# Performance work log

Hardware: AMD Instinct MI355X
Metric: run time of the kernel (lower is better)

Reference implementation:

```python
import math
import jax, jax.numpy as jnp
import numpy as np

N_FEATURES = 32
DEGREE = 3
BATCH = 8192
N_POLY = math.comb(N_FEATURES + DEGREE, DEGREE)  # 6545


def _build_monomial_indices(n_features, degree):
    """Static (numpy) indices replicating the Pascal-triangle recursion in TaylorMap._poly.

    For degree level i (i = 1..degree-1), the original code appends, for each feature f,
    x[:, f] * prev_block[:, :comb(i+f, i)].  We flatten that into gather index arrays so the
    whole block is one vectorized gather+multiply instead of a Python loop of slices/concats.
    """
    levels = []
    for i in range(1, degree):
        counts = np.array([math.comb(i + f, i) for f in range(n_features)], dtype=np.int64)
        f_idx = np.repeat(np.arange(n_features, dtype=np.int64), counts)
        m_idx = np.concatenate([np.arange(c, dtype=np.int64) for c in counts])
        levels.append((f_idx, m_idx))
    return levels

_LEVELS = _build_monomial_indices(N_FEATURES, DEGREE)


def _poly(x):
    # x: [B, n].  Returns [B, n_poly] monomial features in the exact order of TaylorMap._poly.
    b = x.shape[0]
    parts = [jnp.ones((b, 1), x.dtype), x]
    prev = x
    for f_idx, m_idx in _LEVELS:  # static loop over degree levels (degree-1 iterations)
        new = x[:, f_idx] * prev[:, m_idx]  # [B, comb(n+i, i+1)-ish block]
        parts.append(new)
        prev = new
    return jnp.concatenate(parts, axis=-1)


def setup_inputs() -> dict:
    key = jax.random.key(0)
    kx, kw = jax.random.split(key)
    x = jax.random.normal(kx, (BATCH, N_FEATURES), dtype=jnp.float32)
    # learned weight W: [n_poly, n_features] (default init is zeros; use small randn for a
    # non-degenerate numerical baseline)
    W = jax.random.normal(kw, (N_POLY, N_FEATURES), dtype=jnp.float32) * 0.02
    return {"x": x, "W": W}


def reference(x, W):
    # TaylorMap(x) = x * residual + poly(x) @ W   (residual=True)
    return x + _poly(x) @ W
```

## Files before the change

### kernel.cpp

```cpp
#include <hip/hip_runtime.h>
#include <cstdint>
#include <cstddef>
#include <utility>


#define NF 32
#define NPOLY 6545
#define NSTEPS 417
#define NOCT 834
#define TSTRIDE 576
#define D2OFF 40
#define XDSTRIDE 34

typedef _Float16 f16x8 __attribute__((ext_vector_type(8)));
typedef float f32x16 __attribute__((ext_vector_type(16)));

#define D2N 528
struct D2I { uint8_t a[D2N]; uint8_t b[D2N]; };
constexpr D2I build_d2i() {
    D2I t{};
    int k = 0;
    for (int f = 0; f < NF; ++f)
        for (int m = 0; m <= f; ++m) { t.a[k] = (uint8_t)f; t.b[k] = (uint8_t)m; ++k; }
    return t;
}
constexpr D2I D2T = build_d2i();

struct Desc { uint32_t d[NOCT]; };
constexpr Desc build_desc() {
    Desc D{};
    int u = 0;
    for (int o = 0; o < 72; ++o)
        D.d[u++] = (uint32_t)(o * 8);
    for (int f = 0; f < NF; ++f) {
        int cnt = (f + 1) * (f + 2) / 2;
        for (int j8 = 0; j8 < (cnt + 7) / 8; ++j8)
            D.d[u++] = (uint32_t)(D2OFF + 8 * j8) | ((uint32_t)(1 + f) << 16);
    }
    return D;
}
__device__ const Desc DESC_G = build_desc();

struct Oldk { int16_t v[NSTEPS * 16]; };
constexpr Oldk build_oldk() {
    Oldk K{};
    int k = 0;
    for (int ti = 0; ti < 576; ++ti) {
        int old;
        if (ti == 0) old = 0;
        else if (ti <= 32) old = ti;
        else if (ti >= D2OFF && ti < D2OFF + D2N) old = 33 + (ti - D2OFF);
        else old = -1;
        K.v[k++] = (int16_t)old;
    }
    for (int f = 0; f < NF; ++f) {
        int cnt = (f + 1) * (f + 2) / 2;
        int off3 = 0;
        for (int g = 0; g < f; ++g) off3 += (g + 1) * (g + 2) / 2;
        int oc = (cnt + 7) / 8;
        for (int m = 0; m < oc * 8; ++m)
            K.v[k++] = (int16_t)(m < cnt ? 561 + off3 + m : -1);
    }
    return K;
}
__device__ const Oldk OLDK_G = build_oldk();

template<int TI>
__device__ __forceinline__ _Float16 tval(const float (&xr)[NF]) {
    if constexpr (TI == 0) return (_Float16)1.0f;
    else if constexpr (TI >= 1 && TI <= 32) return (_Float16)xr[TI - 1];
    else if constexpr (TI >= D2OFF && TI < D2OFF + D2N) {
        constexpr int m = TI - D2OFF;
        return (_Float16)(xr[D2T.a[m]] * xr[D2T.b[m]]);
    } else return (_Float16)0.0f;
}

template<int O, int... Js>
__device__ __forceinline__ void put_oct(std::integer_sequence<int, Js...>,
                                        const float (&xr)[NF], _Float16* trow, int r) {
    f16x8 v = { tval<O * 8 + Js>(xr)... };
    int slot = (O & ~7) | ((O ^ r) & 7);
    *(f16x8*)(trow + slot * 8) = v;
}

template<int V>
__device__ __forceinline__ void xdw(const float (&xr)[NF], _Float16* xdrow) {
    if constexpr (V == 0) xdrow[0] = (_Float16)1.0f;
    else xdrow[V] = (_Float16)xr[V - 1];
}

template<int G, int... Os>
__device__ __forceinline__ void p1_group(std::integer_sequence<int, Os...>,
                                         const float (&xr)[NF], _Float16* trow,
                                         _Float16* xdrow, int r) {
    (put_oct<9 * G + Os>(std::make_integer_sequence<int, 8>{}, xr, trow, r), ...);
    xdw<4 * G + 0>(xr, xdrow); xdw<4 * G + 1>(xr, xdrow);
    xdw<4 * G + 2>(xr, xdrow); xdw<4 * G + 3>(xr, xdrow);
    if constexpr (G == 7) xdw<32>(xr, xdrow);
}

__global__ void prep(const float* __restrict__ x, const float* __restrict__ W,
                     float* __restrict__ out, _Float16* __restrict__ Wh) {
    int b = blockIdx.x;
    if (b < 256) {
        int id = b * 256 + threadIdx.x;
        ((float4*)out)[id] = ((const float4*)x)[id];
    } else {
        int id = (b - 256) * 256 + threadIdx.x;
        if (id < NSTEPS * 2 * 32) {
            int step = id >> 6, rem = id & 63, hs = rem >> 5, n = rem & 31;
            int k0 = step * 16 + hs * 8;
            f16x8 v;
#pragma unroll
            for (int j = 0; j < 8; ++j) {
                int old = OLDK_G.v[k0 + j];
                v[j] = (_Float16)(old >= 0 ? W[old * 32 + n] : 0.0f);
            }
            *(f16x8*)(Wh + (size_t)id * 8) = v;
        }
    }
}

__global__ __launch_bounds__(256) void gemm(const float* __restrict__ x,
                                            const _Float16* __restrict__ Wh,
                                            float* __restrict__ out) {
    __shared__ __align__(16) unsigned char smem[39040];
    _Float16* t  = (_Float16*)smem;
    _Float16* xd = (_Float16*)(smem + 36864);
    float* red   = (float*)smem;

    const int tid = threadIdx.x;
    const int wave = tid >> 6, lane = tid & 63;
    const int hsel = lane >> 5, r = lane & 31;
    const int mtile = blockIdx.x >> 2, cg = blockIdx.x & 3;

    {
        const int pr = tid & 31, g = tid >> 5;
        float xr[NF];
        const float4* xp = (const float4*)(x + (size_t)(mtile * 32 + pr) * NF);
#pragma unroll
        for (int i = 0; i < 8; ++i) {
            float4 v = xp[i];
            xr[4 * i + 0] = v.x; xr[4 * i + 1] = v.y;
            xr[4 * i + 2] = v.z; xr[4 * i + 3] = v.w;
        }
        _Float16* trow = t + pr * TSTRIDE;
        _Float16* xdrow = xd + pr * XDSTRIDE;
        switch (g) {
            case 0: p1_group<0>(std::make_integer_sequence<int, 9>{}, xr, trow, xdrow, pr); break;
            case 1: p1_group<1>(std::make_integer_sequence<int, 9>{}, xr, trow, xdrow, pr); break;
            case 2: p1_group<2>(std::make_integer_sequence<int, 9>{}, xr, trow, xdrow, pr); break;
            case 3: p1_group<3>(std::make_integer_sequence<int, 9>{}, xr, trow, xdrow, pr); break;
            case 4: p1_group<4>(std::make_integer_sequence<int, 9>{}, xr, trow, xdrow, pr); break;
            case 5: p1_group<5>(std::make_integer_sequence<int, 9>{}, xr, trow, xdrow, pr); break;
            case 6: p1_group<6>(std::make_integer_sequence<int, 9>{}, xr, trow, xdrow, pr); break;
            default: p1_group<7>(std::make_integer_sequence<int, 9>{}, xr, trow, xdrow, pr); break;
        }
    }
    __syncthreads();

    const int c = cg * 4 + wave;
    const int s0 = __builtin_amdgcn_readfirstlane((c * NSTEPS) >> 4);
    const int s1 = __builtin_amdgcn_readfirstlane(((c + 1) * NSTEPS) >> 4);
    const _Float16* trow = t + r * TSTRIDE;
    const _Float16* xdrow = xd + r * XDSTRIDE;
    const _Float16* wp = Wh + (size_t)lane * 8;

    f32x16 acc;
#pragma unroll
    for (int i = 0; i < 16; ++i) acc[i] = 0.0f;

    uint32_t dlo = DESC_G.d[2 * s0];
    uint32_t dhi = DESC_G.d[2 * s0 + 1];
    f16x8 b0 = *(const f16x8*)(wp + (size_t)s0 * 512);
    f16x8 b1 = *(const f16x8*)(wp + (size_t)(s0 + 1) * 512);

    for (int s = s0; s < s1; ++s) {
        uint32_t d = hsel ? dhi : dlo;
        dlo = DESC_G.d[2 * (s + 1)];
        dhi = DESC_G.d[2 * (s + 1) + 1];
        int toff = (int)(d & 0xffffu);
        int xv = (int)(d >> 16);
        int o = toff >> 3;
        int slot = (o & ~7) | ((o ^ r) & 7);
        f16x8 araw = *(const f16x8*)(trow + slot * 8);
        _Float16 xs = xdrow[xv];
        f16x8 xsv = { xs, xs, xs, xs, xs, xs, xs, xs };
        f16x8 a = araw * xsv;
        f16x8 bu = b0; b0 = b1;
        b1 = *(const f16x8*)(wp + (size_t)(s + 2) * 512);
        acc = __builtin_amdgcn_mfma_f32_32x32x16_f16(a, bu, acc, 0, 0, 0);
    }

    __syncthreads();
    float* bank = red + wave * 1024;
#pragma unroll
    for (int reg = 0; reg < 16; ++reg) {
        int rr = (reg & 3) + 8 * (reg >> 2) + 4 * hsel;
        bank[rr * 32 + r] = acc[reg];
    }
    __syncthreads();
    float* op = out + (size_t)mtile * 1024;
#pragma unroll
    for (int i = 0; i < 4; ++i) {
        int e = tid + i * 256;
        float v = red[e] + red[1024 + e] + red[2048 + e] + red[3072 + e];
        atomicAdd(op + e, v);
    }
}

extern "C" void kernel_launch(void* const* d_in, const int* in_sizes, int n_in,
                              void* d_out, int out_size, void* d_ws, size_t ws_size,
                              hipStream_t stream) {
    (void)in_sizes; (void)n_in; (void)out_size; (void)ws_size;
    const float* x = (const float*)d_in[0];
    const float* W = (const float*)d_in[1];
    float* out = (float*)d_out;
    _Float16* Wh = (_Float16*)d_ws;

    prep<<<361, 256, 0, stream>>>(x, W, out, Wh);
    gemm<<<1024, 256, 0, stream>>>(x, Wh, out);
}
```

Baseline: 74.23 us.

## Use one 512-thread block per M-tile, drop atomics, stage descriptors in LDS

The K-split moves from four 256-thread blocks per 32-row tile to a single 512-thread block whose eight waves each take a K slice. Their partials are reduced in LDS and written directly as x plus the sum, which removes the global atomics and the x-to-out copy in the prep kernel. Step descriptors are staged in LDS with byte offsets precomputed. The MFMA loop now alternates two accumulators with deeper software prefetch of A, the scale factor and B. The trade-off is 256 blocks instead of 1024, which lowers grid-level parallelism, and the polynomial tile is rebuilt once per block instead of once per K-group.

```diff
diff --git a/kernel.cpp b/kernel.cpp
--- a/kernel.cpp
+++ b/kernel.cpp
@@ -8,9 +8,17 @@
 #define NPOLY 6545
 #define NSTEPS 417
 #define NOCT 834
+#define NDESC 842
 #define TSTRIDE 576
 #define D2OFF 40
 #define XDSTRIDE 34
+
+#define T_BYTES   36864
+#define XD_OFF    36864
+#define XD_BYTES  2176
+#define DESC_OFF  39040
+#define DESC_BYTES 3368
+#define SMEM_BYTES 42496
 
 typedef _Float16 f16x8 __attribute__((ext_vector_type(8)));
 typedef float f32x16 __attribute__((ext_vector_type(16)));
@@ -31,11 +39,11 @@
     Desc D{};
     int u = 0;
     for (int o = 0; o < 72; ++o)
-        D.d[u++] = (uint32_t)(o * 8);
+        D.d[u++] = (uint32_t)(o * 16);
     for (int f = 0; f < NF; ++f) {
         int cnt = (f + 1) * (f + 2) / 2;
         for (int j8 = 0; j8 < (cnt + 7) / 8; ++j8)
-            D.d[u++] = (uint32_t)(D2OFF + 8 * j8) | ((uint32_t)(1 + f) << 16);
+            D.d[u++] = (uint32_t)((D2OFF + 8 * j8) * 2) | ((uint32_t)((1 + f) * 2) << 16);
     }
     return D;
 }
@@ -83,56 +91,58 @@
     *(f16x8*)(trow + slot * 8) = v;
 }
 
+template<int BASE, int... Os>
+__device__ __forceinline__ void p1_octs(std::integer_sequence<int, Os...>,
+                                        const float (&xr)[NF], _Float16* trow, int r) {
+    (put_oct<BASE + Os>(std::make_integer_sequence<int, 8>{}, xr, trow, r), ...);
+}
+
 template<int V>
 __device__ __forceinline__ void xdw(const float (&xr)[NF], _Float16* xdrow) {
     if constexpr (V == 0) xdrow[0] = (_Float16)1.0f;
-    else xdrow[V] = (_Float16)xr[V - 1];
-}
-
-template<int G, int... Os>
-__device__ __forceinline__ void p1_group(std::integer_sequence<int, Os...>,
-                                         const float (&xr)[NF], _Float16* trow,
+    else if constexpr (V <= 32) xdrow[V] = (_Float16)xr[V - 1];
+}
+
+template<int G>
+__device__ __forceinline__ void p1_group(const float (&xr)[NF], _Float16* trow,
                                          _Float16* xdrow, int r) {
-    (put_oct<9 * G + Os>(std::make_integer_sequence<int, 8>{}, xr, trow, r), ...);
-    xdw<4 * G + 0>(xr, xdrow); xdw<4 * G + 1>(xr, xdrow);
-    xdw<4 * G + 2>(xr, xdrow); xdw<4 * G + 3>(xr, xdrow);
-    if constexpr (G == 7) xdw<32>(xr, xdrow);
-}
-
-__global__ void prep(const float* __restrict__ x, const float* __restrict__ W,
-                     float* __restrict__ out, _Float16* __restrict__ Wh) {
-    int b = blockIdx.x;
-    if (b < 256) {
-        int id = b * 256 + threadIdx.x;
-        ((float4*)out)[id] = ((const float4*)x)[id];
-    } else {
-        int id = (b - 256) * 256 + threadIdx.x;
-        if (id < NSTEPS * 2 * 32) {
-            int step = id >> 6, rem = id & 63, hs = rem >> 5, n = rem & 31;
-            int k0 = step * 16 + hs * 8;
-            f16x8 v;
-#pragma unroll
-            for (int j = 0; j < 8; ++j) {
-                int old = OLDK_G.v[k0 + j];
-                v[j] = (_Float16)(old >= 0 ? W[old * 32 + n] : 0.0f);
-            }
-            *(f16x8*)(Wh + (size_t)id * 8) = v;
+    if constexpr (G < 8)
+        p1_octs<G * 5>(std::make_integer_sequence<int, 5>{}, xr, trow, r);
+    else
+        p1_octs<40 + (G - 8) * 4>(std::make_integer_sequence<int, 4>{}, xr, trow, r);
+    xdw<2 * G>(xr, xdrow);
+    xdw<2 * G + 1>(xr, xdrow);
+    if constexpr (G == 15) xdw<32>(xr, xdrow);
+}
+
+__global__ void prep(const float* __restrict__ W, _Float16* __restrict__ Wh) {
+    int id = blockIdx.x * 256 + threadIdx.x;
+    if (id < NSTEPS * 64) {
+        int step = id >> 6, rem = id & 63, hs = rem >> 5, n = rem & 31;
+        int k0 = step * 16 + hs * 8;
+        f16x8 v;
+#pragma unroll
+        for (int j = 0; j < 8; ++j) {
+            int old = OLDK_G.v[k0 + j];
+            v[j] = (_Float16)(old >= 0 ? W[old * 32 + n] : 0.0f);
         }
-    }
-}
-
-__global__ __launch_bounds__(256) void gemm(const float* __restrict__ x,
-                                            const _Float16* __restrict__ Wh,
-                                            float* __restrict__ out) {
-    __shared__ __align__(16) unsigned char smem[39040];
+        *(f16x8*)(Wh + (size_t)id * 8) = v;
+    }
+}
+
+__global__ __launch_bounds__(512, 2) void gemm(const float* __restrict__ x,
+                                               const _Float16* __restrict__ Wh,
+                                               float* __restrict__ out) {
+    __shared__ __align__(16) unsigned char smem[SMEM_BYTES];
     _Float16* t  = (_Float16*)smem;
-    _Float16* xd = (_Float16*)(smem + 36864);
-    float* red   = (float*)smem;
+    _Float16* xd = (_Float16*)(smem + XD_OFF);
+    uint32_t* descL = (uint32_t*)(smem + DESC_OFF);
 
     const int tid = threadIdx.x;
-    const int wave = tid >> 6, lane = tid & 63;
+    const int wave = __builtin_amdgcn_readfirstlane(tid >> 6);
+    const int lane = tid & 63;
     const int hsel = lane >> 5, r = lane & 31;
-    const int mtile = blockIdx.x >> 2, cg = blockIdx.x & 3;
+    const int mtile = blockIdx.x;
 
     {
         const int pr = tid & 31, g = tid >> 5;
@@ -147,65 +157,89 @@
         _Float16* trow = t + pr * TSTRIDE;
         _Float16* xdrow = xd + pr * XDSTRIDE;
         switch (g) {
-            case 0: p1_group<0>(std::make_integer_sequence<int, 9>{}, xr, trow, xdrow, pr); break;
-            case 1: p1_group<1>(std::make_integer_sequence<int, 9>{}, xr, trow, xdrow, pr); break;
-            case 2: p1_group<2>(std::make_integer_sequence<int, 9>{}, xr, trow, xdrow, pr); break;
-            case 3: p1_group<3>(std::make_integer_sequence<int, 9>{}, xr, trow, xdrow, pr); break;
-            case 4: p1_group<4>(std::make_integer_sequence<int, 9>{}, xr, trow, xdrow, pr); break;
-            case 5: p1_group<5>(std::make_integer_sequence<int, 9>{}, xr, trow, xdrow, pr); break;
-            case 6: p1_group<6>(std::make_integer_sequence<int, 9>{}, xr, trow, xdrow, pr); break;
-            default: p1_group<7>(std::make_integer_sequence<int, 9>{}, xr, trow, xdrow, pr); break;
+            case  0: p1_group< 0>(xr, trow, xdrow, pr); break;
+            case  1: p1_group< 1>(xr, trow, xdrow, pr); break;
+            case  2: p1_group< 2>(xr, trow, xdrow, pr); break;
+            case  3: p1_group< 3>(xr, trow, xdrow, pr); break;
+            case  4: p1_group< 4>(xr, trow, xdrow, pr); break;
+            case  5: p1_group< 5>(xr, trow, xdrow, pr); break;
+            case  6: p1_group< 6>(xr, trow, xdrow, pr); break;
+            case  7: p1_group< 7>(xr, trow, xdrow, pr); break;
+            case  8: p1_group< 8>(xr, trow, xdrow, pr); break;
+            case  9: p1_group< 9>(xr, trow, xdrow, pr); break;
+            case 10: p1_group<10>(xr, trow, xdrow, pr); break;
+            case 11: p1_group<11>(xr, trow, xdrow, pr); break;
+            case 12: p1_group<12>(xr, trow, xdrow, pr); break;
+            case 13: p1_group<13>(xr, trow, xdrow, pr); break;
+            case 14: p1_group<14>(xr, trow, xdrow, pr); break;
+            default: p1_group<15>(xr, trow, xdrow, pr); break;
         }
+#pragma unroll
+        for (int i = tid; i < NDESC; i += 512)
+            descL[i] = (i < NOCT) ? DESC_G.d[i] : 0u;
     }
     __syncthreads();
 
-    const int c = cg * 4 + wave;
-    const int s0 = __builtin_amdgcn_readfirstlane((c * NSTEPS) >> 4);
-    const int s1 = __builtin_amdgcn_readfirstlane(((c + 1) * NSTEPS) >> 4);
-    const _Float16* trow = t + r * TSTRIDE;
-    const _Float16* xdrow = xd + r * XDSTRIDE;
-    const _Float16* wp = Wh + (size_t)lane * 8;
-
-    f32x16 acc;
-#pragma unroll
-    for (int i = 0; i < 16; ++i) acc[i] = 0.0f;
-
-    uint32_t dlo = DESC_G.d[2 * s0];
-    uint32_t dhi = DESC_G.d[2 * s0 + 1];
-    f16x8 b0 = *(const f16x8*)(wp + (size_t)s0 * 512);
-    f16x8 b1 = *(const f16x8*)(wp + (size_t)(s0 + 1) * 512);
-
-    for (int s = s0; s < s1; ++s) {
-        uint32_t d = hsel ? dhi : dlo;
-        dlo = DESC_G.d[2 * (s + 1)];
-        dhi = DESC_G.d[2 * (s + 1) + 1];
-        int toff = (int)(d & 0xffffu);
-        int xv = (int)(d >> 16);
-        int o = toff >> 3;
-        int slot = (o & ~7) | ((o ^ r) & 7);
-        f16x8 araw = *(const f16x8*)(trow + slot * 8);
-        _Float16 xs = xdrow[xv];
-        f16x8 xsv = { xs, xs, xs, xs, xs, xs, xs, xs };
-        f16x8 a = araw * xsv;
-        f16x8 bu = b0; b0 = b1;
-        b1 = *(const f16x8*)(wp + (size_t)(s + 2) * 512);
-        acc = __builtin_amdgcn_mfma_f32_32x32x16_f16(a, bu, acc, 0, 0, 0);
-    }
+    const int s0 = __builtin_amdgcn_readfirstlane((wave * NSTEPS) >> 3);
+    const int s1 = __builtin_amdgcn_readfirstlane(((wave + 1) * NSTEPS) >> 3);
+    const char* trowB = (const char*)t + r * (TSTRIDE * 2);
+    const char* xdrowB = (const char*)xd + r * (XDSTRIDE * 2);
+    const char* wpB = (const char*)Wh + lane * 16;
+    const uint32_t rx = (uint32_t)((r & 7) << 4);
+
+    f32x16 acc0, acc1;
+#pragma unroll
+    for (int i = 0; i < 16; ++i) { acc0[i] = 0.0f; acc1[i] = 0.0f; }
+
+    uint32_t dva = descL[2 * s0 + hsel];
+    uint32_t dvb = descL[2 * s0 + 2 + hsel];
+    f16x8 araw0 = *(const f16x8*)(trowB + ((dva & 0xffffu) ^ rx));
+    _Float16 xs0 = *(const _Float16*)(xdrowB + (dva >> 16));
+    f16x8 araw1 = *(const f16x8*)(trowB + ((dvb & 0xffffu) ^ rx));
+    _Float16 xs1 = *(const _Float16*)(xdrowB + (dvb >> 16));
+    uint32_t dval0 = descL[2 * (s0 + 2) + hsel];
+    uint32_t dval1 = descL[2 * (s0 + 3) + hsel];
+    f16x8 breg0 = *(const f16x8*)(wpB + (size_t)s0 * 1024);
+    f16x8 breg1 = *(const f16x8*)(wpB + (size_t)(s0 + 1) * 1024);
+
+#define BODY(P, SCUR) do {                                                    \
+    uint32_t d_ = dval##P;                                                    \
+    f16x8 xsv_ = { xs##P, xs##P, xs##P, xs##P, xs##P, xs##P, xs##P, xs##P };  \
+    f16x8 a_ = araw##P * xsv_;                                                \
+    f16x8 bu_ = breg##P;                                                      \
+    araw##P = *(const f16x8*)(trowB + ((d_ & 0xffffu) ^ rx));                 \
+    xs##P   = *(const _Float16*)(xdrowB + (d_ >> 16));                        \
+    dval##P = descL[2 * ((SCUR) + 4) + hsel];                                 \
+    breg##P = *(const f16x8*)(wpB + (size_t)((SCUR) + 2) * 1024);             \
+    acc##P = __builtin_amdgcn_mfma_f32_32x32x16_f16(a_, bu_, acc##P, 0, 0, 0);\
+} while (0)
+
+    int s = s0;
+    for (; s + 1 < s1; s += 2) { BODY(0, s); BODY(1, s + 1); }
+    if (s < s1) {
+        f16x8 xsv_ = { xs0, xs0, xs0, xs0, xs0, xs0, xs0, xs0 };
+        f16x8 a_ = araw0 * xsv_;
+        acc0 = __builtin_amdgcn_mfma_f32_32x32x16_f16(a_, breg0, acc0, 0, 0, 0);
+    }
+#undef BODY
 
     __syncthreads();
+    float* red = (float*)smem;
     float* bank = red + wave * 1024;
 #pragma unroll
     for (int reg = 0; reg < 16; ++reg) {
         int rr = (reg & 3) + 8 * (reg >> 2) + 4 * hsel;
-        bank[rr * 32 + r] = acc[reg];
+        bank[rr * 32 + r] = acc0[reg] + acc1[reg];
     }
     __syncthreads();
+    const float* xg = x + (size_t)mtile * 1024;
     float* op = out + (size_t)mtile * 1024;
 #pragma unroll
-    for (int i = 0; i < 4; ++i) {
-        int e = tid + i * 256;
-        float v = red[e] + red[1024 + e] + red[2048 + e] + red[3072 + e];
-        atomicAdd(op + e, v);
+    for (int i = 0; i < 2; ++i) {
+        int e = tid + i * 512;
+        float v = red[e] + red[1024 + e] + red[2048 + e] + red[3072 + e]
+                + red[4096 + e] + red[5120 + e] + red[6144 + e] + red[7168 + e];
+        op[e] = xg[e] + v;
     }
 }
 
@@ -218,6 +252,6 @@
     float* out = (float*)d_out;
     _Float16* Wh = (_Float16*)d_ws;
 
-    prep<<<361, 256, 0, stream>>>(x, W, out, Wh);
-    gemm<<<1024, 256, 0, stream>>>(x, Wh, out);
-}
+    prep<<<105, 256, 0, stream>>>(W, Wh);
+    gemm<<<256, 512, 0, stream>>>(x, Wh, out);
+}
```

Result: faster. 71.00 us (-4.3%).
